# Optimization experiments

Hardware: AMD Instinct MI355X
Metric: run time of the kernel (lower is better)

The kernel has to match this reference:

```python
import jax, jax.numpy as jnp
import numpy as np
import math

B, S, H, NH, NKV, HD = 1, 2048, 4096, 32, 8, 128
ROPE_THETA = 10000.0


def setup_inputs() -> dict:
    key = jax.random.key(0)
    ks = jax.random.split(key, 16)
    hidden_states = jax.random.normal(ks[0], (B, S, H), jnp.float32) * 0.02
    Wq = jax.random.normal(ks[1], (NH * HD, H), jnp.float32) * 0.02
    Wk = jax.random.normal(ks[2], (NKV * HD, H), jnp.float32) * 0.02
    Wv = jax.random.normal(ks[3], (NKV * HD, H), jnp.float32) * 0.02
    Wo = jax.random.normal(ks[4], (H, NH * HD), jnp.float32) * 0.02
    # RoPE cos/sin, HF Llama convention: emb = concat(freqs, freqs)
    inv_freq = 1.0 / (ROPE_THETA ** (jnp.arange(0, HD, 2, dtype=jnp.float32) / HD))
    pos = jnp.arange(S, dtype=jnp.float32)
    freqs = pos[:, None] * inv_freq[None, :]              # [S, HD/2]
    emb = jnp.concatenate([freqs, freqs], axis=-1)        # [S, HD]
    cos = jnp.cos(emb)[None]                              # [1, S, HD]
    sin = jnp.sin(emb)[None]
    # additive causal mask [B, 1, S, S]
    causal = jnp.tril(jnp.ones((S, S), dtype=bool))
    attention_mask = jnp.where(causal, 0.0, -1e9).astype(jnp.float32)[None, None]
    # reorder permutations (as written by GPTQ act-order reordering)
    perm = lambda k, n: jax.random.permutation(k, n).astype(jnp.int32)
    return {
        'hidden_states': hidden_states, 'Wq': Wq, 'Wk': Wk, 'Wv': Wv, 'Wo': Wo,
        'cos': cos, 'sin': sin, 'attention_mask': attention_mask,
        'q_order_col': perm(ks[5], H), 'q_order_row': perm(ks[6], NH * HD),
        'k_order_col': perm(ks[7], H), 'k_order_row': perm(ks[8], NKV * HD),
        'v_order_col': perm(ks[9], H), 'v_order_row': perm(ks[10], NKV * HD),
        'o_order_col': perm(ks[11], NH * HD), 'o_order_row': perm(ks[12], H),
    }


def _rotate_half(x):
    x1, x2 = jnp.split(x, 2, axis=-1)
    return jnp.concatenate([-x2, x1], axis=-1)


def reference(hidden_states, Wq, Wk, Wv, Wo, cos, sin, attention_mask,
              q_order_col, q_order_row, k_order_col, k_order_row,
              v_order_col, v_order_row, o_order_col, o_order_row):
    bsz, q_len, _ = hidden_states.shape
    # permuted projections: gather cols of input, GEMM, gather rows of output
    q = hidden_states[:, :, q_order_col] @ Wq.T
    q = q[:, :, q_order_row]
    k = hidden_states[:, :, k_order_col] @ Wk.T
    k = k[:, :, k_order_row]
    v = hidden_states[:, :, v_order_col] @ Wv.T
    v = v[:, :, v_order_row]
    q = q.reshape(bsz, q_len, NH, HD).transpose(0, 2, 1, 3)   # [B,NH,S,HD]
    k = k.reshape(bsz, q_len, NKV, HD).transpose(0, 2, 1, 3)  # [B,NKV,S,HD]
    v = v.reshape(bsz, q_len, NKV, HD).transpose(0, 2, 1, 3)
    # RoPE
    c = cos[:, None, :, :]  # [1,1,S,HD]
    s = sin[:, None, :, :]
    q = q * c + _rotate_half(q) * s
    k = k * c + _rotate_half(k) * s
    # repeat_kv for GQA
    rep = NH // NKV
    k = jnp.repeat(k, rep, axis=1)  # [B,NH,S,HD]
    v = jnp.repeat(v, rep, axis=1)
    # eager attention: full score matrix, fp32 softmax
    scores = jnp.einsum('bhqd,bhkd->bhqk', q, k) / math.sqrt(HD)
    scores = scores + attention_mask
    probs = jax.nn.softmax(scores.astype(jnp.float32), axis=-1).astype(q.dtype)
    # dropout p=0.0 (eval) -> identity
    attn = jnp.einsum('bhqk,bhkd->bhqd', probs, v)
    attn = attn.transpose(0, 2, 1, 3).reshape(bsz, q_len, NH * HD)
    out = attn[:, :, o_order_col] @ Wo.T
    out = out[:, :, o_order_row]
    return out
```

## Files before the change

### kernel.cpp

```cpp
#include <hip/hip_runtime.h>

typedef unsigned short u16;
typedef unsigned char u8;
typedef __bf16 bf16x8 __attribute__((ext_vector_type(8)));
typedef float f32x4 __attribute__((ext_vector_type(4)));
typedef int i32x4 __attribute__((ext_vector_type(4)));
typedef int i32x8 __attribute__((ext_vector_type(8)));

__device__ __forceinline__ u16 f2bf(float f) {
    unsigned u = __float_as_uint(f);
    unsigned r = (u + 0x7fffu + ((u >> 16) & 1u)) >> 16;
    return (u16)r;
}
__device__ __forceinline__ float bf2f(u16 h) {
    return __uint_as_float(((unsigned)h) << 16);
}
__device__ __forceinline__ unsigned pack_bf2(float lo, float hi) {
    unsigned a = __float_as_uint(hi) + 0x8000u;
    unsigned b = __float_as_uint(lo) + 0x8000u;
    return __builtin_amdgcn_perm(a, b, 0x07060302u);
}
__device__ __forceinline__ unsigned pack_fp8x4(float a, float b, float c, float d) {
    unsigned w = __builtin_amdgcn_cvt_pk_fp8_f32(a, b, 0, false);
    w = __builtin_amdgcn_cvt_pk_fp8_f32(c, d, w, true);
    return w;
}
__device__ __forceinline__ void async_copy16(const void* g, void* l) {
    __builtin_amdgcn_global_load_lds((__attribute__((address_space(1))) void*)(void*)g,
                                     (__attribute__((address_space(3))) void*)l, 16, 0, 0);
}

#define FP8_SCALE 64.0f
#define FP8_UNSCALE (1.0f / 4096.0f)


__global__ void inv4_k(const int* __restrict__ q, const int* __restrict__ k,
                       const int* __restrict__ v, const int* __restrict__ o,
                       int* __restrict__ invq, int* __restrict__ invk,
                       int* __restrict__ invv, int* __restrict__ invo) {
    int i = blockIdx.x * 256 + threadIdx.x;
    int a = i >> 12, j = i & 4095;
    const int* p = a == 0 ? q : a == 1 ? k : a == 2 ? v : o;
    int* inv = a == 0 ? invq : a == 1 ? invk : a == 2 ? invv : invo;
    inv[p[j]] = j;
}

__global__ __launch_bounds__(256) void permw4_k(
    const float* __restrict__ Wq, const float* __restrict__ Wk,
    const float* __restrict__ Wv, const float* __restrict__ Wo,
    const int* __restrict__ qor, const int* __restrict__ kor,
    const int* __restrict__ vor, const int* __restrict__ oor,
    const int* __restrict__ invq, const int* __restrict__ invk,
    const int* __restrict__ invv, const int* __restrict__ invo,
    u8* __restrict__ Wqkf8, u16* __restrict__ Wvp, u16* __restrict__ Wop) {
    __shared__ float rowbuf[4096];
    int j = blockIdx.x;
    const float* W; const int* rp; const int* inv; int row; int f8;
    u8* out8 = nullptr; u16* out16 = nullptr;
    if (j < 4096)      { W = Wq; rp = qor; inv = invq; row = j;        out8 = Wqkf8 + (size_t)j * 4096; f8 = 1; }
    else if (j < 5120) { W = Wk; rp = kor; inv = invk; row = j - 4096; out8 = Wqkf8 + (size_t)j * 4096; f8 = 1; }
    else if (j < 6144) { W = Wv; rp = vor; inv = invv; row = j - 5120; out16 = Wvp + (size_t)(j - 5120) * 4096; f8 = 0; }
    else               { W = Wo; rp = oor; inv = invo; row = j - 6144; out16 = Wop + (size_t)(j - 6144) * 4096; f8 = 0; }
    if (f8) {
        int hd = row & 127, b = hd >> 4;
        row = (row & ~127) | ((hd & 15) | ((b & 1) << 6) | ((b & 2) << 3) | ((hd & 64) >> 1));
    }
    const float4* wr4 = (const float4*)(W + (size_t)rp[row] * 4096);
#pragma unroll
    for (int t = 0; t < 4; t++)
        ((float4*)rowbuf)[threadIdx.x + t * 256] = wr4[threadIdx.x + t * 256];
    __syncthreads();
    if (f8) {
        int t = threadIdx.x;
        const int4* inv4p = (const int4*)inv;
        float v[16];
#pragma unroll
        for (int u = 0; u < 4; u++) {
            int4 ix = inv4p[t * 4 + u];
            v[4 * u + 0] = rowbuf[ix.x] * FP8_SCALE;
            v[4 * u + 1] = rowbuf[ix.y] * FP8_SCALE;
            v[4 * u + 2] = rowbuf[ix.z] * FP8_SCALE;
            v[4 * u + 3] = rowbuf[ix.w] * FP8_SCALE;
        }
        uint4 wv;
        wv.x = pack_fp8x4(v[0], v[1], v[2], v[3]);
        wv.y = pack_fp8x4(v[4], v[5], v[6], v[7]);
        wv.z = pack_fp8x4(v[8], v[9], v[10], v[11]);
        wv.w = pack_fp8x4(v[12], v[13], v[14], v[15]);
        int tb = (t & ~7) | ((t & 7) ^ (j & 7));
        ((uint4*)out8)[tb] = wv;
    } else {
        unsigned* o32 = (unsigned*)out16;
        const int2* inv2 = (const int2*)inv;
#pragma unroll
        for (int t = 0; t < 8; t++) {
            int c = threadIdx.x + t * 256;
            int2 ij = inv2[c];
            o32[c] = pack_bf2(rowbuf[ij.x], rowbuf[ij.y]);
        }
    }
}

__global__ __launch_bounds__(256) void cvt_k(const float* __restrict__ x,
                                             u16* __restrict__ Xb,
                                             u8* __restrict__ Xf8) {
    int row = blockIdx.x;
    int t = threadIdx.x;
    const float4* src = (const float4*)(x + (size_t)row * 4096);
    float v[16];
#pragma unroll
    for (int u = 0; u < 4; u++) {
        float4 a = src[t * 4 + u];
        v[4 * u + 0] = a.x; v[4 * u + 1] = a.y; v[4 * u + 2] = a.z; v[4 * u + 3] = a.w;
    }
    uint4 b0, b1;
    b0.x = pack_bf2(v[0], v[1]);  b0.y = pack_bf2(v[2], v[3]);
    b0.z = pack_bf2(v[4], v[5]);  b0.w = pack_bf2(v[6], v[7]);
    b1.x = pack_bf2(v[8], v[9]);  b1.y = pack_bf2(v[10], v[11]);
    b1.z = pack_bf2(v[12], v[13]); b1.w = pack_bf2(v[14], v[15]);
    uint4* ob = (uint4*)(Xb + (size_t)row * 4096);
    ob[t * 2] = b0;
    ob[t * 2 + 1] = b1;
    uint4 w8;
    w8.x = pack_fp8x4(v[0] * FP8_SCALE, v[1] * FP8_SCALE, v[2] * FP8_SCALE, v[3] * FP8_SCALE);
    w8.y = pack_fp8x4(v[4] * FP8_SCALE, v[5] * FP8_SCALE, v[6] * FP8_SCALE, v[7] * FP8_SCALE);
    w8.z = pack_fp8x4(v[8] * FP8_SCALE, v[9] * FP8_SCALE, v[10] * FP8_SCALE, v[11] * FP8_SCALE);
    w8.w = pack_fp8x4(v[12] * FP8_SCALE, v[13] * FP8_SCALE, v[14] * FP8_SCALE, v[15] * FP8_SCALE);
    int tb = (t & ~7) | ((t & 7) ^ (row & 7));
    ((uint4*)(Xf8 + (size_t)row * 4096))[tb] = w8;
}

__global__ __launch_bounds__(256) void vtr_k(const float* __restrict__ Vpart,
                                             u16* __restrict__ Vt) {
    __shared__ u16 t[64][65];
    int bx = blockIdx.x;
    int s0 = (bx & 31) * 64, c0 = (bx >> 5) * 64;
    int x = threadIdx.x & 63, y4 = threadIdx.x >> 6;
    const float* Vp0 = Vpart;
    const float* Vp1 = Vpart + (size_t)2048 * 1024;
    for (int i = 0; i < 16; i++) {
        int r = y4 * 16 + i;
        size_t idx = (size_t)(s0 + r) * 1024 + c0 + x;
        t[r][x] = f2bf(Vp0[idx] + Vp1[idx]);
    }
    __syncthreads();
    for (int i = 0; i < 16; i++) {
        int r = y4 * 16 + i;
        int xk = 4 * (x & 15) + (x >> 4);
        Vt[(size_t)(c0 + r) * 2048 + s0 + xk] = t[x][r];
    }
}


__global__ __launch_bounds__(256) void gemm_qkv_k(const u8* __restrict__ Xf8,
                                                  const u16* __restrict__ Xb,
                                                  const u8* __restrict__ Wqk,
                                                  const u16* __restrict__ Wv,
                                                  u16* __restrict__ QKV,
                                                  float* __restrict__ Vpart,
                                                  const float* __restrict__ cosv,
                                                  const float* __restrict__ sinv) {
    __shared__ u8 lds[32768];
    const int tid = threadIdx.x;
    const int w = tid >> 6, lane = tid & 63;
    const int quad = lane >> 4, l16 = lane & 15;
    const int bm0 = blockIdx.y * 128;
    const int wm = (w >> 1) * 64, wn = (w & 1) * 64;
    if (blockIdx.x < 40) {
        const int bn0 = blockIdx.x * 128;
        u8* ldsA = lds;
        u8* ldsB = lds + 16384;
        const u8* Ag = Xf8 + (size_t)(bm0 + w * 32 + (lane >> 3)) * 4096 + (lane & 7) * 16;
        const u8* Bg = Wqk + (size_t)(bn0 + w * 32 + (lane >> 3)) * 4096 + (lane & 7) * 16;
        u8* la = ldsA + w * 32 * 128;
        u8* lb = ldsB + w * 32 * 128;
        const int swz = l16 & 7;
        f32x4 acc[4][4] = {};
        for (int k0 = 0; k0 < 4096; k0 += 128) {
#pragma unroll
            for (int t = 0; t < 4; t++) async_copy16(Ag + (size_t)t * 8 * 4096 + k0, la + t * 1024);
#pragma unroll
            for (int t = 0; t < 4; t++) async_copy16(Bg + (size_t)t * 8 * 4096 + k0, lb + t * 1024);
            __syncthreads();
            i32x8 af[4], bf[4];
#pragma unroll
            for (int i = 0; i < 4; i++) {
                int r = wm + i * 16 + l16;
                union { i32x8 v8; i32x4 v4[2]; } u;
                u.v4[0] = *(const i32x4*)&ldsA[r * 128 + ((quad * 2) ^ swz) * 16];
                u.v4[1] = *(const i32x4*)&ldsA[r * 128 + ((quad * 2 + 1) ^ swz) * 16];
                af[i] = u.v8;
            }
#pragma unroll
            for (int j = 0; j < 4; j++) {
                int r = wn + j * 16 + l16;
                union { i32x8 v8; i32x4 v4[2]; } u;
                u.v4[0] = *(const i32x4*)&ldsB[r * 128 + ((quad * 2) ^ swz) * 16];
                u.v4[1] = *(const i32x4*)&ldsB[r * 128 + ((quad * 2 + 1) ^ swz) * 16];
                bf[j] = u.v8;
            }
#pragma unroll
            for (int i = 0; i < 4; i++)
#pragma unroll
                for (int j = 0; j < 4; j++)
                    acc[i][j] = __builtin_amdgcn_mfma_scale_f32_16x16x128_f8f6f4(
                        af[i], bf[j], acc[i][j], 0, 0,
                        0, 0x7F7F7F7F, 0, 0x7F7F7F7F);
            __syncthreads();
        }
        const float qsc = (bn0 < 4096) ? 0.08838834764831845f : 1.0f;
        const int hb = (wn ? 32 : 0) + l16;
#pragma unroll
        for (int i = 0; i < 4; i++) {
            const int row = bm0 + wm + i * 16 + quad * 4;
#pragma unroll
            for (int jp = 0; jp < 2; jp++) {
                const int d1 = hb + jp * 16;
                const int ce = bn0 + wn + jp * 32 + l16;
#pragma unroll
                for (int r = 0; r < 4; r++) {
                    const int s = row + r;
                    const float c  = cosv[s * 128 + d1];
                    const float sn = sinv[s * 128 + d1];
                    const float x1 = acc[i][jp * 2][r]     * FP8_UNSCALE;
                    const float x2 = acc[i][jp * 2 + 1][r] * FP8_UNSCALE;
                    QKV[(size_t)s * 6144 + ce]      = f2bf((x1 * c - x2 * sn) * qsc);
                    QKV[(size_t)s * 6144 + ce + 16] = f2bf((x2 * c + x1 * sn) * qsc);
                }
            }
        }
    } else {
        const int vx = blockIdx.x - 40;
        const int bn0 = (vx & 7) * 128;
        const int kslice = vx >> 3;
        const int kb = kslice * 2048;
        u16* lds_a0 = (u16*)lds;
        u16* lds_a1 = (u16*)(lds + 8192);
        u16* lds_b0 = (u16*)(lds + 16384);
        u16* lds_b1 = (u16*)(lds + 24576);
        const int r0 = w * 16 + (lane >> 2);
        const int c0 = (lane & 3) * 8;
        const u16* Ag = Xb + (size_t)(bm0 + r0) * 4096 + kb + c0;
        const u16* Bg = Wv + (size_t)(bn0 + r0) * 4096 + kb + c0;
        f32x4 acc[4][4] = {};
        for (int k0 = 0; k0 < 2048; k0 += 64) {
            async_copy16(Ag + k0,                         lds_a0 + w * 512);
            async_copy16(Ag + (size_t)64 * 4096 + k0,     lds_a0 + (w + 4) * 512);
            async_copy16(Ag + k0 + 32,                    lds_a1 + w * 512);
            async_copy16(Ag + (size_t)64 * 4096 + k0 + 32, lds_a1 + (w + 4) * 512);
            async_copy16(Bg + k0,                         lds_b0 + w * 512);
            async_copy16(Bg + (size_t)64 * 4096 + k0,     lds_b0 + (w + 4) * 512);
            async_copy16(Bg + k0 + 32,                    lds_b1 + w * 512);
            async_copy16(Bg + (size_t)64 * 4096 + k0 + 32, lds_b1 + (w + 4) * 512);
            __syncthreads();
#pragma unroll
            for (int kk = 0; kk < 2; kk++) {
                const u16* la = kk ? lds_a1 : lds_a0;
                const u16* lb = kk ? lds_b1 : lds_b0;
                bf16x8 af[4], bfv[4];
#pragma unroll
                for (int i = 0; i < 4; i++)
                    af[i] = *(const bf16x8*)&la[(wm + i * 16 + l16) * 32 + quad * 8];
#pragma unroll
                for (int j = 0; j < 4; j++)
                    bfv[j] = *(const bf16x8*)&lb[(wn + j * 16 + l16) * 32 + quad * 8];
#pragma unroll
                for (int i = 0; i < 4; i++)
#pragma unroll
                    for (int j = 0; j < 4; j++)
                        acc[i][j] = __builtin_amdgcn_mfma_f32_16x16x32_bf16(af[i], bfv[j], acc[i][j], 0, 0, 0);
            }
            __syncthreads();
        }
        float* Vp = Vpart + (size_t)kslice * 2048 * 1024;
#pragma unroll
        for (int i = 0; i < 4; i++) {
            const int row = bm0 + wm + i * 16 + quad * 4;
#pragma unroll
            for (int j = 0; j < 4; j++) {
                const int col = bn0 + wn + j * 16 + l16;
#pragma unroll
                for (int r = 0; r < 4; r++)
                    Vp[(size_t)(row + r) * 1024 + col] = acc[i][j][r];
            }
        }
    }
}


__global__ __launch_bounds__(256) void gemm_o_k(const u16* __restrict__ A,
                                                const u16* __restrict__ B,
                                                float* __restrict__ Out) {
    __shared__ u16 lds[16384];
    u16* lds_a0 = lds;
    u16* lds_a1 = lds + 4096;
    u16* lds_b0 = lds + 8192;
    u16* lds_b1 = lds + 12288;
    const int tid = threadIdx.x;
    const int w = tid >> 6, lane = tid & 63;
    const int quad = lane >> 4, l16 = lane & 15;
    const int bm0 = blockIdx.y * 128;
    const int bn0 = (blockIdx.x & 31) * 128;
    const int kslice = blockIdx.x >> 5;
    const int kb = kslice * 2048;
    const int wm = (w >> 1) * 64, wn = (w & 1) * 64;
    const int r0 = w * 16 + (lane >> 2);
    const int c0 = (lane & 3) * 8;
    const u16* Ag = A + (size_t)(bm0 + r0) * 4096 + kb + c0;
    const u16* Bg = B + (size_t)(bn0 + r0) * 4096 + kb + c0;
    f32x4 acc[4][4] = {};
    for (int k0 = 0; k0 < 2048; k0 += 64) {
        async_copy16(Ag + k0,                          lds_a0 + w * 512);
        async_copy16(Ag + (size_t)64 * 4096 + k0,      lds_a0 + (w + 4) * 512);
        async_copy16(Ag + k0 + 32,                     lds_a1 + w * 512);
        async_copy16(Ag + (size_t)64 * 4096 + k0 + 32, lds_a1 + (w + 4) * 512);
        async_copy16(Bg + k0,                          lds_b0 + w * 512);
        async_copy16(Bg + (size_t)64 * 4096 + k0,      lds_b0 + (w + 4) * 512);
        async_copy16(Bg + k0 + 32,                     lds_b1 + w * 512);
        async_copy16(Bg + (size_t)64 * 4096 + k0 + 32, lds_b1 + (w + 4) * 512);
        __syncthreads();
#pragma unroll
        for (int kk = 0; kk < 2; kk++) {
            const u16* la = kk ? lds_a1 : lds_a0;
            const u16* lb = kk ? lds_b1 : lds_b0;
            bf16x8 af[4], bfv[4];
#pragma unroll
            for (int i = 0; i < 4; i++)
                af[i] = *(const bf16x8*)&la[(wm + i * 16 + l16) * 32 + quad * 8];
#pragma unroll
            for (int j = 0; j < 4; j++)
                bfv[j] = *(const bf16x8*)&lb[(wn + j * 16 + l16) * 32 + quad * 8];
#pragma unroll
            for (int i = 0; i < 4; i++)
#pragma unroll
                for (int j = 0; j < 4; j++)
                    acc[i][j] = __builtin_amdgcn_mfma_f32_16x16x32_bf16(af[i], bfv[j], acc[i][j], 0, 0, 0);
        }
        __syncthreads();
    }
#pragma unroll
    for (int i = 0; i < 4; i++) {
        const int row = bm0 + wm + i * 16 + quad * 4;
#pragma unroll
        for (int j = 0; j < 4; j++) {
            const int col = bn0 + wn + j * 16 + l16;
#pragma unroll
            for (int r = 0; r < 4; r++)
                unsafeAtomicAdd(&Out[(size_t)(row + r) * 4096 + col], acc[i][j][r]);
        }
    }
}


__global__ __launch_bounds__(256) void attn_k(const u16* __restrict__ Qb,
                                              const u16* __restrict__ Kb,
                                              const u16* __restrict__ Vt,
                                              u16* __restrict__ Ob,
                                              int qstride, int kstride) {
    __shared__ u16 ldsK[4 * 64 * 32];
    __shared__ u16 ldsV[2 * 128 * 32];
    __shared__ u16 ldsP[4][32 * 72];
    const int h = blockIdx.x;
    const int qt = (int)gridDim.y - 1 - (int)blockIdx.y;
    const int kvh = h >> 2;
    const int tid = threadIdx.x;
    const int w = tid >> 6, lane = tid & 63;
    const int quad = lane >> 4, l16 = lane & 15;
    const int q0 = qt * 128;
    const int wrow = q0 + w * 32;

    bf16x8 qf[2][4];
#pragma unroll
    for (int mi = 0; mi < 2; mi++)
#pragma unroll
        for (int kk = 0; kk < 4; kk++)
            qf[mi][kk] = *(const bf16x8*)&Qb[(size_t)(wrow + mi * 16 + l16) * qstride +
                                             h * 128 + kk * 32 + quad * 8];

    const u16* kp[4]; const u16* vp[4];
    u16* ldk[4]; u16* ldv[4];
#pragma unroll
    for (int t = 0; t < 4; t++) {
        int wl = w + t * 4;
        int kk = wl >> 2, part = wl & 3;
        kp[t] = Kb + (size_t)(part * 16 + (lane >> 2)) * kstride + kvh * 128 + kk * 32 + (lane & 3) * 8;
        int ks2 = wl >> 3, p2 = wl & 7;
        vp[t] = Vt + (size_t)(kvh * 128 + p2 * 16 + (lane >> 2)) * 2048 + ks2 * 32 + (lane & 3) * 8;
        ldk[t] = ldsK + wl * 512;
        ldv[t] = ldsV + wl * 512;
    }

    f32x4 acc_o[2][8] = {};
    float lrow[2][4] = {};

    const int nk = 2 * (qt + 1);
    for (int kn = 0; kn < nk; kn++) {
        const int g0 = kn * 64;
#pragma unroll
        for (int t = 0; t < 4; t++) async_copy16(kp[t], ldk[t]);
#pragma unroll
        for (int t = 0; t < 4; t++) async_copy16(vp[t], ldv[t]);
#pragma unroll
        for (int t = 0; t < 4; t++) { kp[t] += (size_t)64 * kstride; vp[t] += 64; }
        __syncthreads();

        if (g0 <= wrow + 31) {
            f32x4 accs[2][4] = {};
#pragma unroll
            for (int kk = 0; kk < 4; kk++) {
                bf16x8 bfrag[4];
#pragma unroll
                for (int ni = 0; ni < 4; ni++)
                    bfrag[ni] = *(const bf16x8*)&ldsK[kk * 2048 + (ni * 16 + l16) * 32 + quad * 8];
#pragma unroll
                for (int mi = 0; mi < 2; mi++)
#pragma unroll
                    for (int ni = 0; ni < 4; ni++)
                        accs[mi][ni] = __builtin_amdgcn_mfma_f32_16x16x32_bf16(
                            qf[mi][kk], bfrag[ni], accs[mi][ni], 0, 0, 0);
            }
            const bool diag = (g0 + 63 > wrow);
            int kidx[4];
#pragma unroll
            for (int ni = 0; ni < 4; ni++) kidx[ni] = g0 + ni * 16 + l16;
#pragma unroll
            for (int mi = 0; mi < 2; mi++) {
#pragma unroll
                for (int r = 0; r < 4; r++) {
                    const int qrow = wrow + mi * 16 + quad * 4 + r;
                    float p[4];
#pragma unroll
                    for (int ni = 0; ni < 4; ni++) {
                        float s = accs[mi][ni][r];
                        if (diag && (kidx[ni] > qrow)) s = -1e30f;
                        p[ni] = __expf(s);
                    }
                    lrow[mi][r] += (p[0] + p[1]) + (p[2] + p[3]);
                    uint2 pk;
                    pk.x = pack_bf2(p[0], p[1]);
                    pk.y = pack_bf2(p[2], p[3]);
                    *(uint2*)&ldsP[w][(mi * 16 + quad * 4 + r) * 72 + l16 * 4] = pk;
                }
            }
#pragma unroll
            for (int ks = 0; ks < 2; ks++) {
                bf16x8 pa[2];
#pragma unroll
                for (int mi = 0; mi < 2; mi++)
                    pa[mi] = *(const bf16x8*)&ldsP[w][(mi * 16 + l16) * 72 + ks * 32 + quad * 8];
#pragma unroll
                for (int oj = 0; oj < 8; oj++) {
                    bf16x8 vb = *(const bf16x8*)&ldsV[ks * 4096 + (oj * 16 + l16) * 32 + quad * 8];
#pragma unroll
                    for (int mi = 0; mi < 2; mi++)
                        acc_o[mi][oj] = __builtin_amdgcn_mfma_f32_16x16x32_bf16(
                            pa[mi], vb, acc_o[mi][oj], 0, 0, 0);
                }
            }
        }
        __syncthreads();
    }
#pragma unroll
    for (int mi = 0; mi < 2; mi++)
#pragma unroll
        for (int r = 0; r < 4; r++) {
            float l = lrow[mi][r];
            l += __shfl_xor(l, 1);
            l += __shfl_xor(l, 2);
            l += __shfl_xor(l, 4);
            l += __shfl_xor(l, 8);
            const float inv = 1.0f / l;
            const int qrow = wrow + mi * 16 + quad * 4 + r;
#pragma unroll
            for (int oj = 0; oj < 8; oj++)
                Ob[(size_t)qrow * 4096 + h * 128 + oj * 16 + l16] =
                    f2bf(acc_o[mi][oj][r] * inv);
        }
}


extern "C" void kernel_launch(void* const* d_in, const int* in_sizes, int n_in,
                              void* d_out, int out_size, void* d_ws, size_t ws_size,
                              hipStream_t stream) {
    (void)in_sizes; (void)n_in; (void)out_size; (void)ws_size;
    const float* hidden = (const float*)d_in[0];
    const float* Wq = (const float*)d_in[1];
    const float* Wk = (const float*)d_in[2];
    const float* Wv = (const float*)d_in[3];
    const float* Wo = (const float*)d_in[4];
    const float* cosv = (const float*)d_in[5];
    const float* sinv = (const float*)d_in[6];
    const int* qoc = (const int*)d_in[8];
    const int* qor = (const int*)d_in[9];
    const int* koc = (const int*)d_in[10];
    const int* kor = (const int*)d_in[11];
    const int* voc = (const int*)d_in[12];
    const int* vor = (const int*)d_in[13];
    const int* ooc = (const int*)d_in[14];
    const int* oor = (const int*)d_in[15];

    char* ws = (char*)d_ws;
    size_t off = 0;
    int* invq = (int*)(ws + off); off += 16384;
    int* invk = (int*)(ws + off); off += 16384;
    int* invv = (int*)(ws + off); off += 16384;
    int* invo = (int*)(ws + off); off += 16384;
    u16* Wop   = (u16*)(ws + off); off += (size_t)4096 * 4096 * 2;
    u16* Xb    = (u16*)(ws + off); off += (size_t)2048 * 4096 * 2;
    u8*  Wqkf8 = (u8*)(ws + off);  off += (size_t)5120 * 4096;
    u16* Wvp   = (u16*)(ws + off); off += (size_t)1024 * 4096 * 2;
    u8*  Xf8   = (u8*)(ws + off);  off += (size_t)2048 * 4096;
    u16* QKVb  = (u16*)(ws + off); off += (size_t)2048 * 6144 * 2;
    u16* Vtb   = (u16*)(ws + off); off += (size_t)1024 * 2048 * 2;
    float* Vpart = (float*)(ws + off); off += (size_t)2 * 2048 * 1024 * 4;
    u16* Attb  = Xb;

    inv4_k<<<64, 256, 0, stream>>>(qoc, koc, voc, ooc, invq, invk, invv, invo);
    permw4_k<<<10240, 256, 0, stream>>>(Wq, Wk, Wv, Wo, qor, kor, vor, oor,
                                        invq, invk, invv, invo, Wqkf8, Wvp, Wop);
    cvt_k<<<2048, 256, 0, stream>>>(hidden, Xb, Xf8);

    gemm_qkv_k<<<dim3(56, 16), 256, 0, stream>>>(Xf8, Xb, Wqkf8, Wvp, QKVb, Vpart,
                                                 cosv, sinv);

    vtr_k<<<512, 256, 0, stream>>>(Vpart, Vtb);

    attn_k<<<dim3(32, 16), 256, 0, stream>>>(QKVb, QKVb + 4096, Vtb, Attb, 6144, 6144);

    hipMemsetAsync(d_out, 0, (size_t)2048 * 4096 * sizeof(float), stream);
    gemm_o_k<<<dim3(64, 16), 256, 0, stream>>>(Attb, Wop, (float*)d_out);
}
```

Before: 528.6 us.

## Rewrite output GEMM with triple-buffered LDS pipeline and drop split-K atomics

Rewrites the O-projection GEMM to use 256x128 tiles with 512 threads and a three-stage async-copy LDS ring buffer, waiting on partial vmcnt so global loads overlap MFMA work. It XOR-swizzles the LDS layout to avoid bank conflicts and remaps workgroups for L2 locality. It also replaces the split-K atomic accumulation with direct stores, which removes the output memset and the atomic traffic. In exchange, each block now runs the full K loop with fewer blocks (256), which may leave compute units underused. It needs 144KB of dynamic shared memory.

```diff
diff --git a/kernel.cpp b/kernel.cpp
--- a/kernel.cpp
+++ b/kernel.cpp
@@ -288,56 +288,113 @@
 }
 
 
-__global__ __launch_bounds__(256) void gemm_o_k(const u16* __restrict__ A,
-                                                const u16* __restrict__ B,
-                                                float* __restrict__ Out) {
-    __shared__ u16 lds[16384];
-    u16* lds_a0 = lds;
-    u16* lds_a1 = lds + 4096;
-    u16* lds_b0 = lds + 8192;
-    u16* lds_b1 = lds + 12288;
+#define GO_STAGE(bufi, kt) do {                                                   \
+    u16* la_ = S + (bufi) * 24576;                                                \
+    u16* lb_ = la_ + 16384;                                                       \
+    const int k0_ = (kt) * 64;                                                    \
+    _Pragma("unroll")                                                             \
+    for (int u = 0; u < 4; u++)                                                   \
+        async_copy16(Asrc + (size_t)u * 64 * 4096 + k0_, la_ + u * 4096 + sdst);  \
+    _Pragma("unroll")                                                             \
+    for (int u = 0; u < 2; u++)                                                   \
+        async_copy16(Bsrc + (size_t)u * 64 * 4096 + k0_, lb_ + u * 4096 + sdst);  \
+} while (0)
+
+#define GO_COMPUTE(bufi) do {                                                     \
+    const u16* la_ = S + (bufi) * 24576;                                          \
+    const u16* lb_ = la_ + 16384;                                                 \
+    bf16x8 bfr[4][2], afr[2][2];                                                  \
+    _Pragma("unroll")                                                             \
+    for (int j = 0; j < 4; j++) {                                                 \
+        const int rb_ = (wn + j * 16 + l16) * 64;                                 \
+        bfr[j][0] = *(const bf16x8*)&lb_[rb_ + o0];                               \
+        bfr[j][1] = *(const bf16x8*)&lb_[rb_ + o1];                               \
+    }                                                                             \
+    _Pragma("unroll")                                                             \
+    for (int i = 0; i < 2; i++) {                                                 \
+        const int ra_ = (wm + i * 16 + l16) * 64;                                 \
+        afr[i][0] = *(const bf16x8*)&la_[ra_ + o0];                               \
+        afr[i][1] = *(const bf16x8*)&la_[ra_ + o1];                               \
+    }                                                                             \
+    asm volatile("s_waitcnt lgkmcnt(0)" ::: "memory");                            \
+    __builtin_amdgcn_sched_barrier(0);                                            \
+    __builtin_amdgcn_s_setprio(1);                                                \
+    _Pragma("unroll")                                                             \
+    for (int i = 0; i < 2; i++)                                                   \
+        _Pragma("unroll")                                                         \
+        for (int j = 0; j < 4; j++) {                                             \
+            acc[i][j] = __builtin_amdgcn_mfma_f32_16x16x32_bf16(afr[i][0], bfr[j][0], acc[i][j], 0, 0, 0); \
+            acc[i][j] = __builtin_amdgcn_mfma_f32_16x16x32_bf16(afr[i][1], bfr[j][1], acc[i][j], 0, 0, 0); \
+        }                                                                         \
+    __builtin_amdgcn_s_setprio(0);                                                \
+    _Pragma("unroll")                                                             \
+    for (int i = 0; i < 2; i++) {                                                 \
+        const int ra_ = (wm + (i + 2) * 16 + l16) * 64;                           \
+        afr[i][0] = *(const bf16x8*)&la_[ra_ + o0];                               \
+        afr[i][1] = *(const bf16x8*)&la_[ra_ + o1];                               \
+    }                                                                             \
+    asm volatile("s_waitcnt lgkmcnt(0)" ::: "memory");                            \
+    __builtin_amdgcn_sched_barrier(0);                                            \
+    __builtin_amdgcn_s_setprio(1);                                                \
+    _Pragma("unroll")                                                             \
+    for (int i = 0; i < 2; i++)                                                   \
+        _Pragma("unroll")                                                         \
+        for (int j = 0; j < 4; j++) {                                             \
+            acc[i + 2][j] = __builtin_amdgcn_mfma_f32_16x16x32_bf16(afr[i][0], bfr[j][0], acc[i + 2][j], 0, 0, 0); \
+            acc[i + 2][j] = __builtin_amdgcn_mfma_f32_16x16x32_bf16(afr[i][1], bfr[j][1], acc[i + 2][j], 0, 0, 0); \
+        }                                                                         \
+    __builtin_amdgcn_s_setprio(0);                                                \
+} while (0)
+
+#define GO_BAR() asm volatile("s_barrier" ::: "memory")
+
+__global__ __launch_bounds__(512, 2) void gemm_o_k(const u16* __restrict__ A,
+                                                   const u16* __restrict__ B,
+                                                   float* __restrict__ Out) {
+    extern __shared__ u16 S[];
     const int tid = threadIdx.x;
     const int w = tid >> 6, lane = tid & 63;
     const int quad = lane >> 4, l16 = lane & 15;
-    const int bm0 = blockIdx.y * 128;
-    const int bn0 = (blockIdx.x & 31) * 128;
-    const int kslice = blockIdx.x >> 5;
-    const int kb = kslice * 2048;
-    const int wm = (w >> 1) * 64, wn = (w & 1) * 64;
-    const int r0 = w * 16 + (lane >> 2);
-    const int c0 = (lane & 3) * 8;
-    const u16* Ag = A + (size_t)(bm0 + r0) * 4096 + kb + c0;
-    const u16* Bg = B + (size_t)(bn0 + r0) * 4096 + kb + c0;
+    const int linear = blockIdx.y * 32 + blockIdx.x;
+    const int wgid = (linear & 7) * 32 + (linear >> 3);
+    const int bm0 = (wgid >> 5) * 256;
+    const int bn0 = (wgid & 31) * 128;
+    const int wm = (w >> 1) * 64;
+    const int wn = (w & 1) * 64;
+    const int sr = tid >> 3;
+    const int scg = ((tid & 7) ^ (sr & 7)) * 8;
+    const int sdst = tid * 8;
+    const u16* Asrc = A + (size_t)(bm0 + sr) * 4096 + scg;
+    const u16* Bsrc = B + (size_t)(bn0 + sr) * 4096 + scg;
+    const int swz = l16 & 7;
+    const int o0 = (quad ^ swz) * 8;
+    const int o1 = ((4 | quad) ^ swz) * 8;
+
     f32x4 acc[4][4] = {};
-    for (int k0 = 0; k0 < 2048; k0 += 64) {
-        async_copy16(Ag + k0,                          lds_a0 + w * 512);
-        async_copy16(Ag + (size_t)64 * 4096 + k0,      lds_a0 + (w + 4) * 512);
-        async_copy16(Ag + k0 + 32,                     lds_a1 + w * 512);
-        async_copy16(Ag + (size_t)64 * 4096 + k0 + 32, lds_a1 + (w + 4) * 512);
-        async_copy16(Bg + k0,                          lds_b0 + w * 512);
-        async_copy16(Bg + (size_t)64 * 4096 + k0,      lds_b0 + (w + 4) * 512);
-        async_copy16(Bg + k0 + 32,                     lds_b1 + w * 512);
-        async_copy16(Bg + (size_t)64 * 4096 + k0 + 32, lds_b1 + (w + 4) * 512);
-        __syncthreads();
-#pragma unroll
-        for (int kk = 0; kk < 2; kk++) {
-            const u16* la = kk ? lds_a1 : lds_a0;
-            const u16* lb = kk ? lds_b1 : lds_b0;
-            bf16x8 af[4], bfv[4];
-#pragma unroll
-            for (int i = 0; i < 4; i++)
-                af[i] = *(const bf16x8*)&la[(wm + i * 16 + l16) * 32 + quad * 8];
-#pragma unroll
-            for (int j = 0; j < 4; j++)
-                bfv[j] = *(const bf16x8*)&lb[(wn + j * 16 + l16) * 32 + quad * 8];
-#pragma unroll
-            for (int i = 0; i < 4; i++)
-#pragma unroll
-                for (int j = 0; j < 4; j++)
-                    acc[i][j] = __builtin_amdgcn_mfma_f32_16x16x32_bf16(af[i], bfv[j], acc[i][j], 0, 0, 0);
-        }
-        __syncthreads();
-    }
+
+    GO_STAGE(0, 0);
+    GO_STAGE(1, 1);
+    GO_STAGE(2, 2);
+    asm volatile("s_waitcnt vmcnt(12)" ::: "memory");
+    GO_BAR();
+
+    int cur = 0;
+    for (int t = 0; t < 61; ++t) {
+        GO_COMPUTE(cur);
+        GO_BAR();
+        GO_STAGE(cur, t + 3);
+        asm volatile("s_waitcnt vmcnt(12)" ::: "memory");
+        GO_BAR();
+        cur = (cur == 2) ? 0 : cur + 1;
+    }
+    GO_COMPUTE(1);
+    asm volatile("s_waitcnt vmcnt(6)" ::: "memory");
+    GO_BAR();
+    GO_COMPUTE(2);
+    asm volatile("s_waitcnt vmcnt(0)" ::: "memory");
+    GO_BAR();
+    GO_COMPUTE(0);
+
 #pragma unroll
     for (int i = 0; i < 4; i++) {
         const int row = bm0 + wm + i * 16 + quad * 4;
@@ -346,7 +403,7 @@
             const int col = bn0 + wn + j * 16 + l16;
 #pragma unroll
             for (int r = 0; r < 4; r++)
-                unsafeAtomicAdd(&Out[(size_t)(row + r) * 4096 + col], acc[i][j][r]);
+                Out[(size_t)(row + r) * 4096 + col] = acc[i][j][r];
         }
     }
 }
@@ -527,6 +584,5 @@
 
     attn_k<<<dim3(32, 16), 256, 0, stream>>>(QKVb, QKVb + 4096, Vtb, Attb, 6144, 6144);
 
-    hipMemsetAsync(d_out, 0, (size_t)2048 * 4096 * sizeof(float), stream);
-    gemm_o_k<<<dim3(64, 16), 256, 0, stream>>>(Attb, Wop, (float*)d_out);
-}
+    gemm_o_k<<<dim3(32, 8), 512, 147456, stream>>>(Attb, Wop, (float*)d_out);
+}
```

Result: faster. 485.3 us (-8.2%).
